# Kernel tuning notes

Hardware: AMD Instinct MI355X
Metric: run time of the kernel (lower is better)

Reference implementation:

```python
import jax, jax.numpy as jnp
import numpy as np

N_HEADS = 8
N_GROUPS = 32  # GroupNorm groups (normalization(channels) in guided-diffusion)
EPS = 1e-5


def setup_inputs() -> dict:
    key = jax.random.key(0)
    ks = jax.random.split(key, 7)
    b, c, hh, ww = 16, 512, 32, 32
    x = jax.random.normal(ks[0], (b, c, hh, ww), dtype=jnp.float32)
    norm_w = 1.0 + 0.02 * jax.random.normal(ks[1], (c,), dtype=jnp.float32)
    norm_b = 0.02 * jax.random.normal(ks[2], (c,), dtype=jnp.float32)
    # pointwise Conv1d == matmul over channels; note proj_out is zero-initialized
    # in the original, we use random weights so the op is non-trivial.
    qkv_w = jax.random.normal(ks[3], (3 * c, c), dtype=jnp.float32) / np.sqrt(c).astype(np.float32)
    qkv_b = 0.02 * jax.random.normal(ks[4], (3 * c,), dtype=jnp.float32)
    proj_w = jax.random.normal(ks[5], (c, c), dtype=jnp.float32) / np.sqrt(c).astype(np.float32)
    proj_b = 0.02 * jax.random.normal(ks[6], (c,), dtype=jnp.float32)
    return {"x": x, "norm_w": norm_w, "norm_b": norm_b,
            "qkv_w": qkv_w, "qkv_b": qkv_b, "proj_w": proj_w, "proj_b": proj_b}


def reference(x, norm_w, norm_b, qkv_w, qkv_b, proj_w, proj_b):
    b, c, hh, ww = x.shape
    t = hh * ww
    xf = x.reshape(b, c, t)

    # GroupNorm(32, c): normalize over (c//G channels, T) per group
    xg = xf.reshape(b, N_GROUPS, (c // N_GROUPS) * t)
    mu = jnp.mean(xg, axis=-1, keepdims=True)
    var = jnp.var(xg, axis=-1, keepdims=True)
    hn = ((xg - mu) * jax.lax.rsqrt(var + EPS)).reshape(b, c, t)
    hn = hn * norm_w[:, None] + norm_b[:, None]

    # pointwise conv: [b, 3c, t]
    qkv = jnp.einsum('oc,bct->bot', qkv_w, hn) + qkv_b[:, None]

    ch = c // N_HEADS
    qkv = qkv.reshape(b * N_HEADS, 3 * ch, t)
    q, k, v = jnp.split(qkv, 3, axis=1)  # each [b*H, ch, t]
    scale = np.float32(1.0 / np.sqrt(np.sqrt(ch)))
    w = jnp.einsum('bct,bcs->bts', q * scale, k * scale)  # [b*H, t, t]
    w = jax.nn.softmax(w.astype(jnp.float32), axis=-1).astype(qkv.dtype)
    a = jnp.einsum('bts,bcs->bct', w, v).reshape(b, c, t)

    h = jnp.einsum('oc,bct->bot', proj_w, a) + proj_b[:, None]
    return (xf + h).reshape(b, c, hh, ww)
```

## Files before the change

kernel.cpp:

```cpp
#include <hip/hip_runtime.h>

#define TPB 256

typedef __attribute__((ext_vector_type(8))) __bf16 bf16x8;
typedef __attribute__((ext_vector_type(4))) float f32x4;
typedef __attribute__((ext_vector_type(8))) unsigned short u16x8;
typedef __attribute__((ext_vector_type(4))) unsigned short u16x4;
typedef __attribute__((ext_vector_type(4))) unsigned int u32x4;
typedef __attribute__((ext_vector_type(2))) unsigned int u32x2;

typedef __attribute__((address_space(1))) const void gconst_void;
typedef __attribute__((address_space(3))) void lds_void;

__device__ __forceinline__ unsigned short f2bf(float f) {
  unsigned u = __builtin_bit_cast(unsigned, f);
  u += 0x7FFFu + ((u >> 16) & 1u);
  return (unsigned short)(u >> 16);
}

__device__ __forceinline__ float exp2_fast(float x) {
  float r;
  asm("v_exp_f32 %0, %1" : "=v"(r) : "v"(x));
  return r;
}

__device__ __forceinline__ float rcp_fast(float x) {
  float r;
  asm("v_rcp_f32 %0, %1" : "=v"(r) : "v"(x));
  return r;
}

__device__ __forceinline__ unsigned cvt_pk_bf16(float lo, float hi) {
  unsigned r;
  asm("v_cvt_pk_bf16_f32 %0, %1, %2" : "=v"(r) : "v"(lo), "v"(hi));
  return r;
}

__global__ void k_gn_stats(const float* __restrict__ x, float* __restrict__ mu,
                           float* __restrict__ rs) {
  int bg = blockIdx.x;
  const float4* p = reinterpret_cast<const float4*>(x + (size_t)bg * 16384);
  float s = 0.f, ss = 0.f;
  for (int i = threadIdx.x; i < 4096; i += TPB) {
    float4 v = p[i];
    s += v.x + v.y + v.z + v.w;
    ss += v.x * v.x + v.y * v.y + v.z * v.z + v.w * v.w;
  }
#pragma unroll
  for (int off = 1; off < 64; off <<= 1) {
    s += __shfl_xor(s, off, 64);
    ss += __shfl_xor(ss, off, 64);
  }
  __shared__ float rbuf[4][2];
  int wave = threadIdx.x >> 6;
  if ((threadIdx.x & 63) == 0) { rbuf[wave][0] = s; rbuf[wave][1] = ss; }
  __syncthreads();
  if (threadIdx.x == 0) {
    float S = 0.f, SS = 0.f;
    for (int i = 0; i < 4; ++i) { S += rbuf[i][0]; SS += rbuf[i][1]; }
    float m = S * (1.f / 16384.f);
    float var = SS * (1.f / 16384.f) - m * m;
    mu[bg] = m;
    rs[bg] = rsqrtf(var + 1e-5f);
  }
}

__global__ void k_gn_apply(const float* __restrict__ x, const float* __restrict__ mu,
                           const float* __restrict__ rs, const float* __restrict__ nw,
                           const float* __restrict__ nb, unsigned short* __restrict__ hnT) {
  __shared__ unsigned short tile[64][72];
  int b = blockIdx.z, ct = blockIdx.y, tt = blockIdx.x;
  int tid = threadIdx.x;
  int cloc = tid >> 2;
  int tseg = tid & 3;
  int c = ct * 64 + cloc;
  int g = c >> 4;
  float m = mu[b * 32 + g], r = rs[b * 32 + g];
  float a = r * nw[c];
  float bb = nb[c] - m * a;
  const float4* src = reinterpret_cast<const float4*>(
      x + ((size_t)(b * 512 + c)) * 1024 + tt * 64 + tseg * 16);
#pragma unroll
  for (int i = 0; i < 4; ++i) {
    float4 v = src[i];
    int tl = tseg * 16 + i * 4;
    tile[tl + 0][cloc] = f2bf(v.x * a + bb);
    tile[tl + 1][cloc] = f2bf(v.y * a + bb);
    tile[tl + 2][cloc] = f2bf(v.z * a + bb);
    tile[tl + 3][cloc] = f2bf(v.w * a + bb);
  }
  __syncthreads();
  int trow = tid >> 3;
  int cs = (tid & 7) * 8;
#pragma unroll
  for (int p = 0; p < 2; ++p) {
    int tr = trow + p * 32;
    u16x8 v8 = *reinterpret_cast<const u16x8*>(&tile[tr][cs]);
    *reinterpret_cast<u16x8*>(hnT + ((size_t)(b * 1024 + tt * 64 + tr)) * 512 + ct * 64 + cs) = v8;
  }
}

__global__ void k_f32_to_bf16(const float* __restrict__ src, unsigned short* __restrict__ dst,
                              int n4) {
  int i = blockIdx.x * blockDim.x + threadIdx.x;
  if (i < n4) {
    float4 v = reinterpret_cast<const float4*>(src)[i];
    u16x4 o;
    o[0] = f2bf(v.x); o[1] = f2bf(v.y); o[2] = f2bf(v.z); o[3] = f2bf(v.w);
    reinterpret_cast<u16x4*>(dst)[i] = o;
  }
}

__global__ __launch_bounds__(256) void k_qkv_gemm(
    const unsigned short* __restrict__ hnT, const unsigned short* __restrict__ wq,
    const float* __restrict__ qkv_b, unsigned short* __restrict__ Q,
    unsigned short* __restrict__ K, unsigned short* __restrict__ V) {
  __shared__ unsigned short As[2][4096];
  __shared__ unsigned short Bs[2][4096];
  int tid = threadIdx.x;
  int lane = tid & 63, wave = tid >> 6;
  int wm = wave >> 1, wn = wave & 1;
  int g = lane >> 4, li = lane & 15;
  int b = blockIdx.z;
  int mbase = blockIdx.y * 128;
  int nbase = blockIdx.x * 128;

  const unsigned short* Ag = hnT + (size_t)b * 1024 * 512 + (size_t)mbase * 512;
  const unsigned short* Bg = wq + (size_t)nbase * 512;

  int ra = wave * 32 + (lane >> 2);
  int ca = ((lane & 3) ^ (ra & 3)) * 16;
  const char* pA0 = (const char*)Ag + (size_t)ra * 1024 + ca;
  const char* pA1 = pA0 + 16 * 1024;
  const char* pB0 = (const char*)Bg + (size_t)ra * 1024 + ca;
  const char* pB1 = pB0 + 16 * 1024;
  int ldsA0 = (wave * 32) * 32, ldsA1 = (wave * 32 + 16) * 32;

  int swz = ((g * 16) ^ ((li & 3) << 4)) >> 1;

  f32x4 zero = {0.f, 0.f, 0.f, 0.f};
  f32x4 acc[4][4];
#pragma unroll
  for (int mi = 0; mi < 4; ++mi)
#pragma unroll
    for (int ni = 0; ni < 4; ++ni) acc[mi][ni] = zero;

#define GISSUE(k0, buf)                                                                  \
  do {                                                                                   \
    __builtin_amdgcn_global_load_lds((gconst_void*)(pA0 + (k0) * 2),                     \
                                     (lds_void*)&As[buf][ldsA0], 16, 0, 0);              \
    __builtin_amdgcn_global_load_lds((gconst_void*)(pA1 + (k0) * 2),                     \
                                     (lds_void*)&As[buf][ldsA1], 16, 0, 0);              \
    __builtin_amdgcn_global_load_lds((gconst_void*)(pB0 + (k0) * 2),                     \
                                     (lds_void*)&Bs[buf][ldsA0], 16, 0, 0);              \
    __builtin_amdgcn_global_load_lds((gconst_void*)(pB1 + (k0) * 2),                     \
                                     (lds_void*)&Bs[buf][ldsA1], 16, 0, 0);              \
  } while (0)

  GISSUE(0, 0);
  for (int kk = 0; kk < 16; ++kk) {
    int cur = kk & 1;
    __syncthreads();
    if (kk < 15) GISSUE((kk + 1) * 32, cur ^ 1);
    bf16x8 af[4], bfr[4];
#pragma unroll
    for (int mi = 0; mi < 4; ++mi)
      af[mi] = *reinterpret_cast<const bf16x8*>(&As[cur][(wm * 64 + mi * 16 + li) * 32 + swz]);
#pragma unroll
    for (int ni = 0; ni < 4; ++ni)
      bfr[ni] = *reinterpret_cast<const bf16x8*>(&Bs[cur][(wn * 64 + ni * 16 + li) * 32 + swz]);
#pragma unroll
    for (int mi = 0; mi < 4; ++mi)
#pragma unroll
      for (int ni = 0; ni < 4; ++ni)
        acc[mi][ni] = __builtin_amdgcn_mfma_f32_16x16x32_bf16(af[mi], bfr[ni], acc[mi][ni], 0, 0, 0);
  }
#undef GISSUE

  const float SCALE = 0.42466090143f;
#pragma unroll
  for (int ni = 0; ni < 4; ++ni) {
    int o = nbase + wn * 64 + ni * 16 + li;
    int h = o / 192;
    int j = o - h * 192;
    int bh = b * 8 + h;
    float bias = qkv_b[o];
#pragma unroll
    for (int mi = 0; mi < 4; ++mi) {
      int t0 = mbase + wm * 64 + mi * 16 + g * 4;
      f32x4 v = acc[mi][ni];
      if (j < 64) {
#pragma unroll
        for (int r = 0; r < 4; ++r)
          Q[((size_t)bh * 1024 + t0 + r) * 64 + j] = f2bf((v[r] + bias) * SCALE);
      } else if (j < 128) {
#pragma unroll
        for (int r = 0; r < 4; ++r)
          K[((size_t)bh * 1024 + t0 + r) * 64 + (j - 64)] = f2bf((v[r] + bias) * SCALE);
      } else {
        u16x4 pv;
#pragma unroll
        for (int r = 0; r < 4; ++r) pv[r] = f2bf(v[r] + bias);
        *reinterpret_cast<u16x4*>(V + ((size_t)bh * 64 + (j - 128)) * 1024 + t0) = pv;
      }
    }
  }
}

__global__ __launch_bounds__(256) void k_attn(
    const unsigned short* __restrict__ Q, const unsigned short* __restrict__ K,
    const unsigned short* __restrict__ V, unsigned short* __restrict__ aT) {
  __shared__ unsigned short Kls[2][4096];
  __shared__ unsigned short Vls[2][4096];
  int tid = threadIdx.x;
  int lane = tid & 63, w = tid >> 6;
  int g = lane >> 4, li = lane & 15;
  int bh = blockIdx.y;
  int tq0 = blockIdx.x * 128;
  int b = bh >> 3, h = bh & 7;

  const unsigned short* Kg = K + (size_t)bh * 1024 * 64;
  const unsigned short* Vg = V + (size_t)bh * 64 * 1024;

  bf16x8 qf[2][2];
#pragma unroll
  for (int qi = 0; qi < 2; ++qi) {
    int t = tq0 + w * 32 + qi * 16 + li;
    const unsigned short* qp = Q + ((size_t)bh * 1024 + t) * 64 + g * 8;
    qf[qi][0] = *reinterpret_cast<const bf16x8*>(qp);
    qf[qi][1] = *reinterpret_cast<const bf16x8*>(qp + 32);
  }

  int r0 = w * 16 + (lane >> 3);
  int r1 = r0 + 8;
  int h0 = (r0 ^ (r0 >> 2)) & 7;
  int h1 = (r1 ^ (r1 >> 2)) & 7;
  int c0 = ((lane & 7) ^ h0) * 8;
  int c1 = ((lane & 7) ^ h1) * 8;
  const unsigned short* kg0 = Kg + (size_t)r0 * 64 + c0;
  const unsigned short* kg1 = Kg + (size_t)r1 * 64 + c1;
  const unsigned short* vg0 = Vg + (size_t)r0 * 1024 + c0;
  const unsigned short* vg1 = Vg + (size_t)r1 * 1024 + c1;

  int srowK = ((li >> 2) << 3) | (li & 3);

  f32x4 zero = {0.f, 0.f, 0.f, 0.f};
  f32x4 oacc[2][4];
  f32x4 l_acc[2];
#pragma unroll
  for (int qi = 0; qi < 2; ++qi) {
    l_acc[qi] = zero;
#pragma unroll
    for (int nj = 0; nj < 4; ++nj) oacc[qi][nj] = zero;
  }
  u32x4 onesw = {0x3F803F80u, 0x3F803F80u, 0x3F803F80u, 0x3F803F80u};
  bf16x8 ones = __builtin_bit_cast(bf16x8, onesw);

#define ISSUE(tt, pp)                                                                    \
  do {                                                                                   \
    __builtin_amdgcn_global_load_lds((gconst_void*)(kg0 + (size_t)(tt) * 4096),          \
                                     (lds_void*)&Kls[pp][w * 1024], 16, 0, 0);           \
    __builtin_amdgcn_global_load_lds((gconst_void*)(kg1 + (size_t)(tt) * 4096),          \
                                     (lds_void*)&Kls[pp][w * 1024 + 512], 16, 0, 0);     \
    __builtin_amdgcn_global_load_lds((gconst_void*)(vg0 + (size_t)(tt) * 64),            \
                                     (lds_void*)&Vls[pp][w * 1024], 16, 0, 0);           \
    __builtin_amdgcn_global_load_lds((gconst_void*)(vg1 + (size_t)(tt) * 64),            \
                                     (lds_void*)&Vls[pp][w * 1024 + 512], 16, 0, 0);     \
  } while (0)

  ISSUE(0, 0);

  for (int t = 0; t < 16; ++t) {
    int cur = t & 1;
    __syncthreads();
    if (t < 15) ISSUE(t + 1, cur ^ 1);

    f32x4 sacc[2][4];
#pragma unroll
    for (int ni = 0; ni < 4; ++ni) {
      int rK = ((ni >> 1) << 5) + ((ni & 1) << 2) + srowK;
      int hs = ((rK ^ (rK >> 2)) & 7) << 4;
      int off0 = ((0 << 6) + (g << 4)) ^ hs;
      int off1 = ((1 << 6) + (g << 4)) ^ hs;
      bf16x8 kf0 = *reinterpret_cast<const bf16x8*>(&Kls[cur][rK * 64 + (off0 >> 1)]);
      bf16x8 kf1 = *reinterpret_cast<const bf16x8*>(&Kls[cur][rK * 64 + (off1 >> 1)]);
#pragma unroll
      for (int qi = 0; qi < 2; ++qi) {
        f32x4 s0 = __builtin_amdgcn_mfma_f32_16x16x32_bf16(kf0, qf[qi][0], zero, 0, 0, 0);
        sacc[qi][ni] = __builtin_amdgcn_mfma_f32_16x16x32_bf16(kf1, qf[qi][1], s0, 0, 0, 0);
      }
    }

    bf16x8 pfrag[2][2];
#pragma unroll
    for (int qi = 0; qi < 2; ++qi) {
#pragma unroll
      for (int ni = 0; ni < 4; ++ni)
#pragma unroll
        for (int r = 0; r < 4; ++r) sacc[qi][ni][r] = exp2_fast(sacc[qi][ni][r]);
#pragma unroll
      for (int kk = 0; kk < 2; ++kk) {
        u32x4 pw;
        pw[0] = cvt_pk_bf16(sacc[qi][2 * kk][0], sacc[qi][2 * kk][1]);
        pw[1] = cvt_pk_bf16(sacc[qi][2 * kk][2], sacc[qi][2 * kk][3]);
        pw[2] = cvt_pk_bf16(sacc[qi][2 * kk + 1][0], sacc[qi][2 * kk + 1][1]);
        pw[3] = cvt_pk_bf16(sacc[qi][2 * kk + 1][2], sacc[qi][2 * kk + 1][3]);
        pfrag[qi][kk] = __builtin_bit_cast(bf16x8, pw);
      }
      l_acc[qi] = __builtin_amdgcn_mfma_f32_16x16x32_bf16(ones, pfrag[qi][0], l_acc[qi], 0, 0, 0);
      l_acc[qi] = __builtin_amdgcn_mfma_f32_16x16x32_bf16(ones, pfrag[qi][1], l_acc[qi], 0, 0, 0);
    }

#pragma unroll
    for (int nj = 0; nj < 4; ++nj) {
      int rV = nj * 16 + li;
      int hv = ((rV ^ (rV >> 2)) & 7) << 4;
      int off0 = ((0 << 6) + (g << 4)) ^ hv;
      int off1 = ((1 << 6) + (g << 4)) ^ hv;
      bf16x8 vf0 = *reinterpret_cast<const bf16x8*>(&Vls[cur][rV * 64 + (off0 >> 1)]);
      bf16x8 vf1 = *reinterpret_cast<const bf16x8*>(&Vls[cur][rV * 64 + (off1 >> 1)]);
#pragma unroll
      for (int qi = 0; qi < 2; ++qi) {
        oacc[qi][nj] = __builtin_amdgcn_mfma_f32_16x16x32_bf16(vf0, pfrag[qi][0], oacc[qi][nj], 0, 0, 0);
        oacc[qi][nj] = __builtin_amdgcn_mfma_f32_16x16x32_bf16(vf1, pfrag[qi][1], oacc[qi][nj], 0, 0, 0);
      }
    }
  }
#undef ISSUE

#pragma unroll
  for (int qi = 0; qi < 2; ++qi) {
    float inv = rcp_fast(l_acc[qi][0]);
    int t = tq0 + w * 32 + qi * 16 + li;
#pragma unroll
    for (int nj = 0; nj < 4; ++nj) {
      u32x2 ov;
      ov[0] = cvt_pk_bf16(oacc[qi][nj][0] * inv, oacc[qi][nj][1] * inv);
      ov[1] = cvt_pk_bf16(oacc[qi][nj][2] * inv, oacc[qi][nj][3] * inv);
      *reinterpret_cast<u32x2*>(aT + ((size_t)b * 1024 + t) * 512 + h * 64 + nj * 16 + g * 4) = ov;
    }
  }
}

__global__ __launch_bounds__(256) void k_proj_gemm(
    const unsigned short* __restrict__ aT, const unsigned short* __restrict__ wp,
    const float* __restrict__ proj_b, const float* __restrict__ x,
    float* __restrict__ out) {
  __shared__ unsigned short As[2][4096];
  __shared__ unsigned short Bs[2][4096];
  int tid = threadIdx.x;
  int lane = tid & 63, wave = tid >> 6;
  int wm = wave >> 1, wn = wave & 1;
  int g = lane >> 4, li = lane & 15;
  int b = blockIdx.z;
  int mbase = blockIdx.y * 128;
  int nbase = blockIdx.x * 128;

  const unsigned short* Ag = wp + (size_t)mbase * 512;
  const unsigned short* Bg = aT + (size_t)b * 1024 * 512 + (size_t)nbase * 512;

  int ra = wave * 32 + (lane >> 2);
  int ca = ((lane & 3) ^ (ra & 3)) * 16;
  const char* pA0 = (const char*)Ag + (size_t)ra * 1024 + ca;
  const char* pA1 = pA0 + 16 * 1024;
  const char* pB0 = (const char*)Bg + (size_t)ra * 1024 + ca;
  const char* pB1 = pB0 + 16 * 1024;
  int ldsA0 = (wave * 32) * 32, ldsA1 = (wave * 32 + 16) * 32;

  int swz = ((g * 16) ^ ((li & 3) << 4)) >> 1;

  f32x4 zero = {0.f, 0.f, 0.f, 0.f};
  f32x4 acc[4][4];
#pragma unroll
  for (int mi = 0; mi < 4; ++mi)
#pragma unroll
    for (int ni = 0; ni < 4; ++ni) acc[mi][ni] = zero;

#define GISSUE(k0, buf)                                                                  \
  do {                                                                                   \
    __builtin_amdgcn_global_load_lds((gconst_void*)(pA0 + (k0) * 2),                     \
                                     (lds_void*)&As[buf][ldsA0], 16, 0, 0);              \
    __builtin_amdgcn_global_load_lds((gconst_void*)(pA1 + (k0) * 2),                     \
                                     (lds_void*)&As[buf][ldsA1], 16, 0, 0);              \
    __builtin_amdgcn_global_load_lds((gconst_void*)(pB0 + (k0) * 2),                     \
                                     (lds_void*)&Bs[buf][ldsA0], 16, 0, 0);              \
    __builtin_amdgcn_global_load_lds((gconst_void*)(pB1 + (k0) * 2),                     \
                                     (lds_void*)&Bs[buf][ldsA1], 16, 0, 0);              \
  } while (0)

  GISSUE(0, 0);
  for (int kk = 0; kk < 16; ++kk) {
    int cur = kk & 1;
    __syncthreads();
    if (kk < 15) GISSUE((kk + 1) * 32, cur ^ 1);
    bf16x8 af[4], bfr[4];
#pragma unroll
    for (int mi = 0; mi < 4; ++mi)
      af[mi] = *reinterpret_cast<const bf16x8*>(&As[cur][(wm * 64 + mi * 16 + li) * 32 + swz]);
#pragma unroll
    for (int ni = 0; ni < 4; ++ni)
      bfr[ni] = *reinterpret_cast<const bf16x8*>(&Bs[cur][(wn * 64 + ni * 16 + li) * 32 + swz]);
#pragma unroll
    for (int mi = 0; mi < 4; ++mi)
#pragma unroll
      for (int ni = 0; ni < 4; ++ni)
        acc[mi][ni] = __builtin_amdgcn_mfma_f32_16x16x32_bf16(af[mi], bfr[ni], acc[mi][ni], 0, 0, 0);
  }
#undef GISSUE

#pragma unroll
  for (int mi = 0; mi < 4; ++mi) {
#pragma unroll
    for (int ni = 0; ni < 4; ++ni) {
      int t = nbase + wn * 64 + ni * 16 + li;
      f32x4 v = acc[mi][ni];
#pragma unroll
      for (int r = 0; r < 4; ++r) {
        int o = mbase + wm * 64 + mi * 16 + g * 4 + r;
        size_t idx = ((size_t)(b * 512 + o)) * 1024 + t;
        out[idx] = v[r] + proj_b[o] + x[idx];
      }
    }
  }
}

extern "C" void kernel_launch(void* const* d_in, const int* in_sizes, int n_in,
                              void* d_out, int out_size, void* d_ws, size_t ws_size,
                              hipStream_t stream) {
  (void)in_sizes; (void)n_in; (void)out_size; (void)ws_size;
  const float* x = (const float*)d_in[0];
  const float* norm_w = (const float*)d_in[1];
  const float* norm_b = (const float*)d_in[2];
  const float* qkv_w = (const float*)d_in[3];
  const float* qkv_b = (const float*)d_in[4];
  const float* proj_w = (const float*)d_in[5];
  const float* proj_b = (const float*)d_in[6];
  float* out = (float*)d_out;

  char* ws = (char*)d_ws;
  size_t off = 0;
  float* mu = (float*)(ws + off); off += 2048;
  float* rs = (float*)(ws + off); off += 2048;
  unsigned short* hnT = (unsigned short*)(ws + off); off += (size_t)16 * 1024 * 512 * 2;
  unsigned short* wqb = (unsigned short*)(ws + off); off += (size_t)1536 * 512 * 2;
  unsigned short* wpb = (unsigned short*)(ws + off); off += (size_t)512 * 512 * 2;
  unsigned short* Qb = (unsigned short*)(ws + off); off += (size_t)128 * 1024 * 64 * 2;
  unsigned short* Kb = (unsigned short*)(ws + off); off += (size_t)128 * 1024 * 64 * 2;
  unsigned short* Vb = (unsigned short*)(ws + off); off += (size_t)128 * 1024 * 64 * 2;

  k_gn_stats<<<512, TPB, 0, stream>>>(x, mu, rs);
  k_gn_apply<<<dim3(16, 8, 16), TPB, 0, stream>>>(x, mu, rs, norm_w, norm_b, hnT);
  k_f32_to_bf16<<<(786432 / 4 + TPB - 1) / TPB, TPB, 0, stream>>>(qkv_w, wqb, 786432 / 4);
  k_f32_to_bf16<<<(262144 / 4 + TPB - 1) / TPB, TPB, 0, stream>>>(proj_w, wpb, 262144 / 4);
  k_qkv_gemm<<<dim3(12, 8, 16), TPB, 0, stream>>>(hnT, wqb, qkv_b, Qb, Kb, Vb);
  k_attn<<<dim3(8, 128), TPB, 0, stream>>>(Qb, Kb, Vb, hnT );
  k_proj_gemm<<<dim3(8, 4, 16), TPB, 0, stream>>>(hnT, wpb, proj_b, x, out);
}
```

Baseline: 151.4 us.

## Triple-buffer LDS pipelines with vmcnt waits and XCD-aware block remapping

The two GEMMs and the attention kernel move from double to triple LDS buffering, issuing loads two tiles ahead. A full __syncthreads is replaced by a partial s_waitcnt vmcnt plus s_barrier, so the next tile's loads can stay in flight during compute. Grids are flattened to 1D with a remap so that consecutive blocks sharing data land on the same XCD for L2 reuse. The GEMM LDS layout and swizzle are also reworked. The cost is more LDS per block, which may lower occupancy, and the hand-written waitcnt logic depends on exact load counts being correct.

```diff
diff --git a/kernel.cpp b/kernel.cpp
--- a/kernel.cpp
+++ b/kernel.cpp
@@ -115,28 +115,34 @@
     const unsigned short* __restrict__ hnT, const unsigned short* __restrict__ wq,
     const float* __restrict__ qkv_b, unsigned short* __restrict__ Q,
     unsigned short* __restrict__ K, unsigned short* __restrict__ V) {
-  __shared__ unsigned short As[2][4096];
-  __shared__ unsigned short Bs[2][4096];
+  __shared__ unsigned short As[3][4096];
+  __shared__ unsigned short Bs[3][4096];
   int tid = threadIdx.x;
   int lane = tid & 63, wave = tid >> 6;
   int wm = wave >> 1, wn = wave & 1;
   int g = lane >> 4, li = lane & 15;
-  int b = blockIdx.z;
-  int mbase = blockIdx.y * 128;
-  int nbase = blockIdx.x * 128;
+
+  int wg = blockIdx.x;
+  int lin = (wg & 7) * 192 + (wg >> 3);
+  int bx = lin % 12;
+  int tmp = lin / 12;
+  int by = tmp & 7;
+  int b = tmp >> 3;
+  int mbase = by * 128;
+  int nbase = bx * 128;
 
   const unsigned short* Ag = hnT + (size_t)b * 1024 * 512 + (size_t)mbase * 512;
   const unsigned short* Bg = wq + (size_t)nbase * 512;
 
-  int ra = wave * 32 + (lane >> 2);
-  int ca = ((lane & 3) ^ (ra & 3)) * 16;
-  const char* pA0 = (const char*)Ag + (size_t)ra * 1024 + ca;
+  int kq = (lane & 3) ^ ((lane >> 3) & 3);
+  int rst = wave * 32 + (lane >> 2);
+  const char* pA0 = (const char*)Ag + (size_t)rst * 1024 + kq * 16;
   const char* pA1 = pA0 + 16 * 1024;
-  const char* pB0 = (const char*)Bg + (size_t)ra * 1024 + ca;
+  const char* pB0 = (const char*)Bg + (size_t)rst * 1024 + kq * 16;
   const char* pB1 = pB0 + 16 * 1024;
-  int ldsA0 = (wave * 32) * 32, ldsA1 = (wave * 32 + 16) * 32;
-
-  int swz = ((g * 16) ^ ((li & 3) << 4)) >> 1;
+  int ldsA0 = wave * 1024, ldsA1 = wave * 1024 + 512;
+
+  int voff = 32 * li + 8 * (g ^ ((li >> 1) & 3));
 
   f32x4 zero = {0.f, 0.f, 0.f, 0.f};
   f32x4 acc[4][4];
@@ -158,17 +164,24 @@
   } while (0)
 
   GISSUE(0, 0);
+  GISSUE(32, 1);
+#pragma unroll
   for (int kk = 0; kk < 16; ++kk) {
-    int cur = kk & 1;
-    __syncthreads();
-    if (kk < 15) GISSUE((kk + 1) * 32, cur ^ 1);
+    if (kk < 15)
+      asm volatile("s_waitcnt vmcnt(4)" ::: "memory");
+    else
+      asm volatile("s_waitcnt vmcnt(0)" ::: "memory");
+    __builtin_amdgcn_s_barrier();
+    asm volatile("" ::: "memory");
+    if (kk < 14) GISSUE((kk + 2) * 32, (kk + 2) % 3);
+    const int cur = kk % 3;
     bf16x8 af[4], bfr[4];
 #pragma unroll
     for (int mi = 0; mi < 4; ++mi)
-      af[mi] = *reinterpret_cast<const bf16x8*>(&As[cur][(wm * 64 + mi * 16 + li) * 32 + swz]);
+      af[mi] = *reinterpret_cast<const bf16x8*>(&As[cur][wm * 2048 + mi * 512 + voff]);
 #pragma unroll
     for (int ni = 0; ni < 4; ++ni)
-      bfr[ni] = *reinterpret_cast<const bf16x8*>(&Bs[cur][(wn * 64 + ni * 16 + li) * 32 + swz]);
+      bfr[ni] = *reinterpret_cast<const bf16x8*>(&Bs[cur][wn * 2048 + ni * 512 + voff]);
 #pragma unroll
     for (int mi = 0; mi < 4; ++mi)
 #pragma unroll
@@ -210,13 +223,17 @@
 __global__ __launch_bounds__(256) void k_attn(
     const unsigned short* __restrict__ Q, const unsigned short* __restrict__ K,
     const unsigned short* __restrict__ V, unsigned short* __restrict__ aT) {
-  __shared__ unsigned short Kls[2][4096];
-  __shared__ unsigned short Vls[2][4096];
+  __shared__ unsigned short Kls[3][4096];
+  __shared__ unsigned short Vls[3][4096];
   int tid = threadIdx.x;
   int lane = tid & 63, w = tid >> 6;
   int g = lane >> 4, li = lane & 15;
-  int bh = blockIdx.y;
-  int tq0 = blockIdx.x * 128;
+
+  int wg = blockIdx.x;
+  int lin = (wg & 7) * 128 + (wg >> 3);
+  int qt = lin & 7;
+  int bh = lin >> 3;
+  int tq0 = qt * 128;
   int b = bh >> 3, h = bh & 7;
 
   const unsigned short* Kg = K + (size_t)bh * 1024 * 64;
@@ -268,65 +285,71 @@
                                      (lds_void*)&Vls[pp][w * 1024 + 512], 16, 0, 0);     \
   } while (0)
 
+#define ABODY(cur)                                                                        \
+  do {                                                                                    \
+    const unsigned short* kbase = &Kls[cur][0];                                           \
+    const unsigned short* vbase = &Vls[cur][0];                                           \
+    f32x4 sacc[2][4];                                                                     \
+    _Pragma("unroll") for (int ni = 0; ni < 4; ++ni) {                                    \
+      int rK = ((ni >> 1) << 5) + ((ni & 1) << 2) + srowK;                                \
+      int hs = ((rK ^ (rK >> 2)) & 7) << 4;                                               \
+      int off0 = ((g << 4)) ^ hs;                                                         \
+      int off1 = (64 + (g << 4)) ^ hs;                                                    \
+      bf16x8 kf0 = *reinterpret_cast<const bf16x8*>(&kbase[rK * 64 + (off0 >> 1)]);       \
+      bf16x8 kf1 = *reinterpret_cast<const bf16x8*>(&kbase[rK * 64 + (off1 >> 1)]);       \
+      _Pragma("unroll") for (int qi = 0; qi < 2; ++qi) {                                  \
+        f32x4 s0 = __builtin_amdgcn_mfma_f32_16x16x32_bf16(kf0, qf[qi][0], zero, 0, 0, 0);\
+        sacc[qi][ni] = __builtin_amdgcn_mfma_f32_16x16x32_bf16(kf1, qf[qi][1], s0, 0, 0, 0);\
+      }                                                                                   \
+    }                                                                                     \
+    bf16x8 pfrag[2][2];                                                                   \
+    _Pragma("unroll") for (int qi = 0; qi < 2; ++qi) {                                    \
+      _Pragma("unroll") for (int ni = 0; ni < 4; ++ni)                                    \
+        _Pragma("unroll") for (int r = 0; r < 4; ++r)                                     \
+          sacc[qi][ni][r] = exp2_fast(sacc[qi][ni][r]);                                   \
+      _Pragma("unroll") for (int kk = 0; kk < 2; ++kk) {                                  \
+        u32x4 pw;                                                                         \
+        pw[0] = cvt_pk_bf16(sacc[qi][2 * kk][0], sacc[qi][2 * kk][1]);                    \
+        pw[1] = cvt_pk_bf16(sacc[qi][2 * kk][2], sacc[qi][2 * kk][3]);                    \
+        pw[2] = cvt_pk_bf16(sacc[qi][2 * kk + 1][0], sacc[qi][2 * kk + 1][1]);            \
+        pw[3] = cvt_pk_bf16(sacc[qi][2 * kk + 1][2], sacc[qi][2 * kk + 1][3]);            \
+        pfrag[qi][kk] = __builtin_bit_cast(bf16x8, pw);                                   \
+      }                                                                                   \
+      l_acc[qi] = __builtin_amdgcn_mfma_f32_16x16x32_bf16(ones, pfrag[qi][0], l_acc[qi], 0, 0, 0); \
+      l_acc[qi] = __builtin_amdgcn_mfma_f32_16x16x32_bf16(ones, pfrag[qi][1], l_acc[qi], 0, 0, 0); \
+    }                                                                                     \
+    _Pragma("unroll") for (int nj = 0; nj < 4; ++nj) {                                    \
+      int rV = nj * 16 + li;                                                              \
+      int hv = ((rV ^ (rV >> 2)) & 7) << 4;                                               \
+      int off0 = ((g << 4)) ^ hv;                                                         \
+      int off1 = (64 + (g << 4)) ^ hv;                                                    \
+      bf16x8 vf0 = *reinterpret_cast<const bf16x8*>(&vbase[rV * 64 + (off0 >> 1)]);       \
+      bf16x8 vf1 = *reinterpret_cast<const bf16x8*>(&vbase[rV * 64 + (off1 >> 1)]);       \
+      _Pragma("unroll") for (int qi = 0; qi < 2; ++qi) {                                  \
+        oacc[qi][nj] = __builtin_amdgcn_mfma_f32_16x16x32_bf16(vf0, pfrag[qi][0], oacc[qi][nj], 0, 0, 0); \
+        oacc[qi][nj] = __builtin_amdgcn_mfma_f32_16x16x32_bf16(vf1, pfrag[qi][1], oacc[qi][nj], 0, 0, 0); \
+      }                                                                                   \
+    }                                                                                     \
+  } while (0)
+
   ISSUE(0, 0);
-
-  for (int t = 0; t < 16; ++t) {
-    int cur = t & 1;
-    __syncthreads();
-    if (t < 15) ISSUE(t + 1, cur ^ 1);
-
-    f32x4 sacc[2][4];
-#pragma unroll
-    for (int ni = 0; ni < 4; ++ni) {
-      int rK = ((ni >> 1) << 5) + ((ni & 1) << 2) + srowK;
-      int hs = ((rK ^ (rK >> 2)) & 7) << 4;
-      int off0 = ((0 << 6) + (g << 4)) ^ hs;
-      int off1 = ((1 << 6) + (g << 4)) ^ hs;
-      bf16x8 kf0 = *reinterpret_cast<const bf16x8*>(&Kls[cur][rK * 64 + (off0 >> 1)]);
-      bf16x8 kf1 = *reinterpret_cast<const bf16x8*>(&Kls[cur][rK * 64 + (off1 >> 1)]);
-#pragma unroll
-      for (int qi = 0; qi < 2; ++qi) {
-        f32x4 s0 = __builtin_amdgcn_mfma_f32_16x16x32_bf16(kf0, qf[qi][0], zero, 0, 0, 0);
-        sacc[qi][ni] = __builtin_amdgcn_mfma_f32_16x16x32_bf16(kf1, qf[qi][1], s0, 0, 0, 0);
-      }
-    }
-
-    bf16x8 pfrag[2][2];
-#pragma unroll
-    for (int qi = 0; qi < 2; ++qi) {
-#pragma unroll
-      for (int ni = 0; ni < 4; ++ni)
-#pragma unroll
-        for (int r = 0; r < 4; ++r) sacc[qi][ni][r] = exp2_fast(sacc[qi][ni][r]);
-#pragma unroll
-      for (int kk = 0; kk < 2; ++kk) {
-        u32x4 pw;
-        pw[0] = cvt_pk_bf16(sacc[qi][2 * kk][0], sacc[qi][2 * kk][1]);
-        pw[1] = cvt_pk_bf16(sacc[qi][2 * kk][2], sacc[qi][2 * kk][3]);
-        pw[2] = cvt_pk_bf16(sacc[qi][2 * kk + 1][0], sacc[qi][2 * kk + 1][1]);
-        pw[3] = cvt_pk_bf16(sacc[qi][2 * kk + 1][2], sacc[qi][2 * kk + 1][3]);
-        pfrag[qi][kk] = __builtin_bit_cast(bf16x8, pw);
-      }
-      l_acc[qi] = __builtin_amdgcn_mfma_f32_16x16x32_bf16(ones, pfrag[qi][0], l_acc[qi], 0, 0, 0);
-      l_acc[qi] = __builtin_amdgcn_mfma_f32_16x16x32_bf16(ones, pfrag[qi][1], l_acc[qi], 0, 0, 0);
-    }
-
-#pragma unroll
-    for (int nj = 0; nj < 4; ++nj) {
-      int rV = nj * 16 + li;
-      int hv = ((rV ^ (rV >> 2)) & 7) << 4;
-      int off0 = ((0 << 6) + (g << 4)) ^ hv;
-      int off1 = ((1 << 6) + (g << 4)) ^ hv;
-      bf16x8 vf0 = *reinterpret_cast<const bf16x8*>(&Vls[cur][rV * 64 + (off0 >> 1)]);
-      bf16x8 vf1 = *reinterpret_cast<const bf16x8*>(&Vls[cur][rV * 64 + (off1 >> 1)]);
-#pragma unroll
-      for (int qi = 0; qi < 2; ++qi) {
-        oacc[qi][nj] = __builtin_amdgcn_mfma_f32_16x16x32_bf16(vf0, pfrag[qi][0], oacc[qi][nj], 0, 0, 0);
-        oacc[qi][nj] = __builtin_amdgcn_mfma_f32_16x16x32_bf16(vf1, pfrag[qi][1], oacc[qi][nj], 0, 0, 0);
-      }
-    }
-  }
+  ISSUE(1, 1);
+  int cur = 0, ib = 2;
+  for (int t = 0; t < 15; ++t) {
+    asm volatile("s_waitcnt vmcnt(4)" ::: "memory");
+    __builtin_amdgcn_s_barrier();
+    asm volatile("" ::: "memory");
+    if (t < 14) ISSUE(t + 2, ib);
+    ABODY(cur);
+    cur = (cur == 2) ? 0 : cur + 1;
+    ib = (ib == 2) ? 0 : ib + 1;
+  }
+  asm volatile("s_waitcnt vmcnt(0)" ::: "memory");
+  __builtin_amdgcn_s_barrier();
+  asm volatile("" ::: "memory");
+  ABODY(cur);
 #undef ISSUE
+#undef ABODY
 
 #pragma unroll
   for (int qi = 0; qi < 2; ++qi) {
@@ -346,28 +369,34 @@
     const unsigned short* __restrict__ aT, const unsigned short* __restrict__ wp,
     const float* __restrict__ proj_b, const float* __restrict__ x,
     float* __restrict__ out) {
-  __shared__ unsigned short As[2][4096];
-  __shared__ unsigned short Bs[2][4096];
+  __shared__ unsigned short As[3][4096];
+  __shared__ unsigned short Bs[3][4096];
   int tid = threadIdx.x;
   int lane = tid & 63, wave = tid >> 6;
   int wm = wave >> 1, wn = wave & 1;
   int g = lane >> 4, li = lane & 15;
-  int b = blockIdx.z;
-  int mbase = blockIdx.y * 128;
-  int nbase = blockIdx.x * 128;
+
+  int wg = blockIdx.x;
+  int lin = (wg & 7) * 64 + (wg >> 3);
+  int bx = lin & 7;
+  int tmp = lin >> 3;
+  int by = tmp & 3;
+  int b = tmp >> 2;
+  int mbase = by * 128;
+  int nbase = bx * 128;
 
   const unsigned short* Ag = wp + (size_t)mbase * 512;
   const unsigned short* Bg = aT + (size_t)b * 1024 * 512 + (size_t)nbase * 512;
 
-  int ra = wave * 32 + (lane >> 2);
-  int ca = ((lane & 3) ^ (ra & 3)) * 16;
-  const char* pA0 = (const char*)Ag + (size_t)ra * 1024 + ca;
+  int kq = (lane & 3) ^ ((lane >> 3) & 3);
+  int rst = wave * 32 + (lane >> 2);
+  const char* pA0 = (const char*)Ag + (size_t)rst * 1024 + kq * 16;
   const char* pA1 = pA0 + 16 * 1024;
-  const char* pB0 = (const char*)Bg + (size_t)ra * 1024 + ca;
+  const char* pB0 = (const char*)Bg + (size_t)rst * 1024 + kq * 16;
   const char* pB1 = pB0 + 16 * 1024;
-  int ldsA0 = (wave * 32) * 32, ldsA1 = (wave * 32 + 16) * 32;
-
-  int swz = ((g * 16) ^ ((li & 3) << 4)) >> 1;
+  int ldsA0 = wave * 1024, ldsA1 = wave * 1024 + 512;
+
+  int voff = 32 * li + 8 * (g ^ ((li >> 1) & 3));
 
   f32x4 zero = {0.f, 0.f, 0.f, 0.f};
   f32x4 acc[4][4];
@@ -389,17 +418,24 @@
   } while (0)
 
   GISSUE(0, 0);
+  GISSUE(32, 1);
+#pragma unroll
   for (int kk = 0; kk < 16; ++kk) {
-    int cur = kk & 1;
-    __syncthreads();
-    if (kk < 15) GISSUE((kk + 1) * 32, cur ^ 1);
+    if (kk < 15)
+      asm volatile("s_waitcnt vmcnt(4)" ::: "memory");
+    else
+      asm volatile("s_waitcnt vmcnt(0)" ::: "memory");
+    __builtin_amdgcn_s_barrier();
+    asm volatile("" ::: "memory");
+    if (kk < 14) GISSUE((kk + 2) * 32, (kk + 2) % 3);
+    const int cur = kk % 3;
     bf16x8 af[4], bfr[4];
 #pragma unroll
     for (int mi = 0; mi < 4; ++mi)
-      af[mi] = *reinterpret_cast<const bf16x8*>(&As[cur][(wm * 64 + mi * 16 + li) * 32 + swz]);
+      af[mi] = *reinterpret_cast<const bf16x8*>(&As[cur][wm * 2048 + mi * 512 + voff]);
 #pragma unroll
     for (int ni = 0; ni < 4; ++ni)
-      bfr[ni] = *reinterpret_cast<const bf16x8*>(&Bs[cur][(wn * 64 + ni * 16 + li) * 32 + swz]);
+      bfr[ni] = *reinterpret_cast<const bf16x8*>(&Bs[cur][wn * 2048 + ni * 512 + voff]);
 #pragma unroll
     for (int mi = 0; mi < 4; ++mi)
 #pragma unroll
@@ -452,7 +488,7 @@
   k_gn_apply<<<dim3(16, 8, 16), TPB, 0, stream>>>(x, mu, rs, norm_w, norm_b, hnT);
   k_f32_to_bf16<<<(786432 / 4 + TPB - 1) / TPB, TPB, 0, stream>>>(qkv_w, wqb, 786432 / 4);
   k_f32_to_bf16<<<(262144 / 4 + TPB - 1) / TPB, TPB, 0, stream>>>(proj_w, wpb, 262144 / 4);
-  k_qkv_gemm<<<dim3(12, 8, 16), TPB, 0, stream>>>(hnT, wqb, qkv_b, Qb, Kb, Vb);
-  k_attn<<<dim3(8, 128), TPB, 0, stream>>>(Qb, Kb, Vb, hnT );
-  k_proj_gemm<<<dim3(8, 4, 16), TPB, 0, stream>>>(hnT, wpb, proj_b, x, out);
-}
+  k_qkv_gemm<<<1536, TPB, 0, stream>>>(hnT, wqb, qkv_b, Qb, Kb, Vb);
+  k_attn<<<1024, TPB, 0, stream>>>(Qb, Kb, Vb, hnT );
+  k_proj_gemm<<<512, TPB, 0, stream>>>(hnT, wpb, proj_b, x, out);
+}
```

Measured after the change: 142.3 us. 6.1% less time.
